# Optimization experiments

Measured on AMD Instinct MI355X. Metric: run time of the kernel, lower is better.

Reference implementation:

```python
import jax, jax.numpy as jnp
import numpy as np

B, T, C, H = 2, 2048, 1024, 16
D = C // H  # head dim = 64

def setup_inputs() -> dict:
    key = jax.random.key(0)
    ks = jax.random.split(key, 6)
    s = 0.02
    return {
        "x":  jax.random.normal(ks[0], (B, T, C), dtype=jnp.float32),
        "Wk": jax.random.normal(ks[1], (C, C), dtype=jnp.float32) * s,
        "Wq": jax.random.normal(ks[2], (C, C), dtype=jnp.float32) * s,
        "Wv": jax.random.normal(ks[3], (C, C), dtype=jnp.float32) * s,
        "Wp": jax.random.normal(ks[4], (C, C), dtype=jnp.float32) * s,
        "bp": jax.random.normal(ks[5], (C,), dtype=jnp.float32) * s,
    }

def reference(x, Wk, Wq, Wv, Wp, bp):
    Bs, Ts, Cs = x.shape
    # torch Linear: y = x @ W.T  (W is [out, in])
    def proj_heads(W):
        p = jnp.einsum('btc,dc->btd', x, W)
        return p.reshape(Bs, Ts, H, D).transpose(0, 2, 1, 3)  # [B,H,T,D]
    k = proj_heads(Wk)
    q = proj_heads(Wq)
    v = proj_heads(Wv)
    scale = 1.0 / jnp.sqrt(jnp.asarray(D, dtype=x.dtype))
    att = jnp.einsum('bhtd,bhsd->bhts', q, k) * scale  # [B,H,T,T]
    att = jax.nn.softmax(att, axis=-1)  # NOTE: no causal mask in the original forward
    y = jnp.einsum('bhts,bhsd->bhtd', att, v)
    y = y.transpose(0, 2, 1, 3).reshape(Bs, Ts, Cs)
    return jnp.einsum('btc,dc->btd', y, Wp) + bp
```

## Files before the change

### kernel.cpp

```cpp
#include <hip/hip_runtime.h>
#include <hip/hip_bf16.h>


typedef __bf16 bf16x8 __attribute__((ext_vector_type(8)));
typedef __bf16 bf16x4 __attribute__((ext_vector_type(4)));
typedef float  f32x4  __attribute__((ext_vector_type(4)));
typedef unsigned int uint2v __attribute__((ext_vector_type(2)));

#define QSCALE 0.18033688011112042f

__device__ __forceinline__ void gload_lds16(const void* g, void* l) {
  __builtin_amdgcn_global_load_lds((const __attribute__((address_space(1))) void*)g,
                                   (__attribute__((address_space(3))) void*)l, 16, 0, 0);
}
__device__ __forceinline__ unsigned int lds_off(const void* p) {
  return (unsigned int)(uintptr_t)(__attribute__((address_space(3))) const char*)p;
}
template<int IMM>
__device__ __forceinline__ uint2v tr_b64(unsigned int addr) {
  uint2v r;
  asm volatile("ds_read_b64_tr_b16 %0, %1 offset:%2" : "=v"(r) : "v"(addr), "i"(IMM));
  return r;
}

__global__ __launch_bounds__(256) void cvt_bf16(
    const float* __restrict__ x,  const float* __restrict__ wq, const float* __restrict__ wk,
    const float* __restrict__ wv, const float* __restrict__ wp,
    __bf16* __restrict__ xb,  __bf16* __restrict__ wqb, __bf16* __restrict__ wkb,
    __bf16* __restrict__ wvb, __bf16* __restrict__ wpb) {
  long long i = ((long long)blockIdx.x * 256 + threadIdx.x) * 4;
  const float* src; __bf16* dst; long long off;
  if      (i < 4194304LL) { src = x;  dst = xb;  off = i; }
  else if (i < 5242880LL) { src = wq; dst = wqb; off = i - 4194304LL; }
  else if (i < 6291456LL) { src = wk; dst = wkb; off = i - 5242880LL; }
  else if (i < 7340032LL) { src = wv; dst = wvb; off = i - 6291456LL; }
  else                    { src = wp; dst = wpb; off = i - 7340032LL; }
  float4 v = *(const float4*)(src + off);
  bf16x4 o;
  o[0] = (__bf16)v.x; o[1] = (__bf16)v.y; o[2] = (__bf16)v.z; o[3] = (__bf16)v.w;
  *(bf16x4*)(dst + off) = o;
}

__device__ __forceinline__ void gemm_core_128(
    const __bf16* __restrict__ A, const __bf16* __restrict__ Bw,
    int tileM, int tileN, char* smA, char* smB, f32x4 acc[4][4]) {
  const int tid = threadIdx.x;
  const int lane = tid & 63;
  const int wid = tid >> 6;
  const int wr = wid >> 1, wc = wid & 1;
  #pragma unroll 1
  for (int k0 = 0; k0 < 1024; k0 += 64) {
    __syncthreads();
    #pragma unroll
    for (int r = 0; r < 4; ++r) {
      int ci = tid + 256 * r;
      int row = ci >> 3, c = ci & 7;
      int sc = (c ^ (row & 7)) * 8;
      gload_lds16(A  + (long long)(tileM + row) * 1024 + k0 + sc, smA + ci * 16);
      gload_lds16(Bw + (long long)(tileN + row) * 1024 + k0 + sc, smB + ci * 16);
    }
    __syncthreads();
    #pragma unroll
    for (int kk = 0; kk < 2; ++kk) {
      bf16x8 af[4], bfr[4];
      #pragma unroll
      for (int i = 0; i < 4; ++i) {
        int mrow = wr * 64 + i * 16 + (lane & 15);
        af[i]  = *(const bf16x8*)(smA + mrow * 128 +
                   ((kk * 64 + (lane >> 4) * 16) ^ ((mrow & 7) << 4)));
        int nrow = wc * 64 + i * 16 + (lane & 15);
        bfr[i] = *(const bf16x8*)(smB + nrow * 128 +
                   ((kk * 64 + (lane >> 4) * 16) ^ ((nrow & 7) << 4)));
      }
      __builtin_amdgcn_s_setprio(1);
      #pragma unroll
      for (int mi = 0; mi < 4; ++mi)
        #pragma unroll
        for (int ni = 0; ni < 4; ++ni)
          acc[mi][ni] = __builtin_amdgcn_mfma_f32_16x16x32_bf16(af[mi], bfr[ni], acc[mi][ni], 0, 0, 0);
      __builtin_amdgcn_s_setprio(0);
    }
  }
}

__global__ __launch_bounds__(256) void gemm_qkv(
    const __bf16* __restrict__ Xb, const __bf16* __restrict__ Wqb,
    const __bf16* __restrict__ Wkb, const __bf16* __restrict__ Wvb,
    __bf16* __restrict__ Qh, __bf16* __restrict__ Kh, __bf16* __restrict__ Vh) {
  __shared__ __align__(16) char smA[16384];
  __shared__ __align__(16) char smB[16384];
  const int z = blockIdx.z;
  const __bf16* W = (z == 0) ? Wqb : (z == 1) ? Wkb : Wvb;
  __bf16* dst     = (z == 0) ? Qh  : (z == 1) ? Kh  : Vh;
  const float scale = (z == 0) ? QSCALE : 1.0f;
  const int tileM = blockIdx.x * 128, tileN = blockIdx.y * 128;
  f32x4 acc[4][4] = {};
  gemm_core_128(Xb, W, tileM, tileN, smA, smB, acc);
  const int lane = threadIdx.x & 63, wid = threadIdx.x >> 6;
  const int wr = wid >> 1, wc = wid & 1;
  #pragma unroll
  for (int mi = 0; mi < 4; ++mi) {
    #pragma unroll
    for (int ni = 0; ni < 4; ++ni) {
      int n = tileN + wc * 64 + ni * 16 + (lane & 15);
      int h = n >> 6, d = n & 63;
      #pragma unroll
      for (int r = 0; r < 4; ++r) {
        int m = tileM + wr * 64 + mi * 16 + (lane >> 4) * 4 + r;
        int b = m >> 11, t = m & 2047;
        dst[((b * 16 + h) * 2048 + t) * 64 + d] = (__bf16)(acc[mi][ni][r] * scale);
      }
    }
  }
}

__global__ __launch_bounds__(256) void gemm_proj(
    const __bf16* __restrict__ Yb, const __bf16* __restrict__ Wpb,
    const float* __restrict__ bias, float* __restrict__ out) {
  __shared__ __align__(16) char smA[16384];
  __shared__ __align__(16) char smB[16384];
  const int tileM = blockIdx.x * 128, tileN = blockIdx.y * 128;
  f32x4 acc[4][4] = {};
  gemm_core_128(Yb, Wpb, tileM, tileN, smA, smB, acc);
  const int lane = threadIdx.x & 63, wid = threadIdx.x >> 6;
  const int wr = wid >> 1, wc = wid & 1;
  #pragma unroll
  for (int mi = 0; mi < 4; ++mi) {
    #pragma unroll
    for (int ni = 0; ni < 4; ++ni) {
      int n = tileN + wc * 64 + ni * 16 + (lane & 15);
      float bv = bias[n];
      #pragma unroll
      for (int r = 0; r < 4; ++r) {
        int m = tileM + wr * 64 + mi * 16 + (lane >> 4) * 4 + r;
        out[(long long)m * 1024 + n] = acc[mi][ni][r] + bv;
      }
    }
  }
}

template<int KS>
__device__ __forceinline__ void pv_half(const char* Pw, unsigned int trb, int lane,
                                        f32x4 Oa[2][4]) {
  bf16x8 pa[2];
  #pragma unroll
  for (int mi = 0; mi < 2; ++mi) {
    int row = mi * 16 + (lane & 15);
    pa[mi] = *(const bf16x8*)(Pw + row * 128 +
               ((KS * 64 + (lane >> 4) * 16) ^ ((row & 7) << 4)));
  }
  uint2v t0[4], t1[4];
  t0[0] = tr_b64<KS * 1024 + 0 * 2048>(trb);  t1[0] = tr_b64<KS * 1024 + 0 * 2048 + 512>(trb);
  t0[1] = tr_b64<KS * 1024 + 1 * 2048>(trb);  t1[1] = tr_b64<KS * 1024 + 1 * 2048 + 512>(trb);
  t0[2] = tr_b64<KS * 1024 + 2 * 2048>(trb);  t1[2] = tr_b64<KS * 1024 + 2 * 2048 + 512>(trb);
  t0[3] = tr_b64<KS * 1024 + 3 * 2048>(trb);  t1[3] = tr_b64<KS * 1024 + 3 * 2048 + 512>(trb);
  asm volatile("s_waitcnt lgkmcnt(0)");
  __builtin_amdgcn_sched_barrier(0);
  __builtin_amdgcn_s_setprio(1);
  #pragma unroll
  for (int nd = 0; nd < 4; ++nd) {
    uint4 u; u.x = t0[nd][0]; u.y = t0[nd][1]; u.z = t1[nd][0]; u.w = t1[nd][1];
    bf16x8 vf = __builtin_bit_cast(bf16x8, u);
    #pragma unroll
    for (int mi = 0; mi < 2; ++mi)
      Oa[mi][nd] = __builtin_amdgcn_mfma_f32_16x16x32_bf16(pa[mi], vf, Oa[mi][nd], 0, 0, 0);
  }
  __builtin_amdgcn_s_setprio(0);
}

__global__ __launch_bounds__(256) void attn(
    const __bf16* __restrict__ Qh, const __bf16* __restrict__ Kh,
    const __bf16* __restrict__ Vh, float* __restrict__ Opart,
    float* __restrict__ lpart) {
  __shared__ __align__(16) char Ksm[8192];
  __shared__ __align__(16) char Vsm[8192];
  __shared__ __align__(16) char Psm[16384];
  const int tid = threadIdx.x, lane = tid & 63, wid = tid >> 6;
  const int bh = blockIdx.x;
  const int qb = blockIdx.y;
  const int split = blockIdx.z;
  const int base = bh * (2048 * 64);
  const int qrow0 = qb * 128 + wid * 32;
  const int key0 = split * 1024;

  bf16x8 qf[2][2];
  #pragma unroll
  for (int mi = 0; mi < 2; ++mi)
    #pragma unroll
    for (int kk = 0; kk < 2; ++kk)
      qf[mi][kk] = *(const bf16x8*)(Qh + base + (qrow0 + mi * 16 + (lane & 15)) * 64
                                    + kk * 32 + (lane >> 4) * 8);

  f32x4 Oa[2][4] = {};
  f32x4 lsum[2] = {};
  char* Pw = Psm + wid * 4096;
  const unsigned int trb = lds_off(Vsm) + lane * 8;

  const int kst_row = (tid + 0) >> 3;
  (void)kst_row;

  #pragma unroll 1
  for (int kt = 0; kt < 16; ++kt) {
    __syncthreads();
    #pragma unroll
    for (int r = 0; r < 2; ++r) {
      int ci = tid + 256 * r;
      int row = ci >> 3, c = ci & 7;
      int sc = (c ^ (row & 7)) * 8;
      gload_lds16(Kh + base + (key0 + kt * 64 + row) * 64 + sc, Ksm + ci * 16);
    }
    #pragma unroll
    for (int r = 0; r < 2; ++r) {
      int c = wid + 4 * r;
      int ks = c & 1, d4 = c >> 1;
      int key = ks * 32 + ((lane >> 3) & 3) * 8 + ((lane >> 5) & 1) * 4 + ((lane >> 1) & 3);
      int d = d4 * 16 + (lane & 1) * 8;
      gload_lds16(Vh + base + (key0 + kt * 64 + key) * 64 + d,
                  Vsm + ks * 1024 + d4 * 2048 + lane * 16);
    }
    __syncthreads();

    f32x4 S[2][4] = {};
    #pragma unroll
    for (int kk = 0; kk < 2; ++kk) {
      bf16x8 kf[4];
      #pragma unroll
      for (int ni = 0; ni < 4; ++ni) {
        int row = ni * 16 + (lane & 15);
        kf[ni] = *(const bf16x8*)(Ksm + row * 128 +
                   ((kk * 64 + (lane >> 4) * 16) ^ ((row & 7) << 4)));
      }
      __builtin_amdgcn_s_setprio(1);
      #pragma unroll
      for (int mi = 0; mi < 2; ++mi)
        #pragma unroll
        for (int ni = 0; ni < 4; ++ni)
          S[mi][ni] = __builtin_amdgcn_mfma_f32_16x16x32_bf16(qf[mi][kk], kf[ni], S[mi][ni], 0, 0, 0);
      __builtin_amdgcn_s_setprio(0);
    }

    #pragma unroll
    for (int mi = 0; mi < 2; ++mi) {
      #pragma unroll
      for (int ni = 0; ni < 4; ++ni) {
        f32x4 p;
        #pragma unroll
        for (int r = 0; r < 4; ++r) p[r] = exp2f(fminf(S[mi][ni][r], 60.0f));
        lsum[mi] += p;
        int key2 = (ni * 16 + (lane & 15)) * 2;
        #pragma unroll
        for (int r = 0; r < 4; ++r) {
          int row = mi * 16 + (lane >> 4) * 4 + r;
          *(__bf16*)(Pw + row * 128 + (key2 ^ ((row & 7) << 4))) = (__bf16)p[r];
        }
      }
    }

    pv_half<0>(Pw, trb, lane, Oa);
    pv_half<1>(Pw, trb, lane, Oa);
  }

  float* Op = Opart + (long long)(split * 32 + bh) * 2048 * 64;
  float* lp = lpart + (split * 32 + bh) * 2048;
  #pragma unroll
  for (int mi = 0; mi < 2; ++mi) {
    f32x4 ls = lsum[mi];
    #pragma unroll
    for (int off = 1; off < 16; off <<= 1) {
      ls[0] += __shfl_xor(ls[0], off, 64);
      ls[1] += __shfl_xor(ls[1], off, 64);
      ls[2] += __shfl_xor(ls[2], off, 64);
      ls[3] += __shfl_xor(ls[3], off, 64);
    }
    #pragma unroll
    for (int r = 0; r < 4; ++r) {
      int t = qrow0 + mi * 16 + (lane >> 4) * 4 + r;
      if ((lane & 15) == 0) lp[t] = ls[r];
      #pragma unroll
      for (int nd = 0; nd < 4; ++nd)
        Op[(long long)t * 64 + nd * 16 + (lane & 15)] = Oa[mi][nd][r];
    }
  }
}

__global__ __launch_bounds__(256) void attn_combine(
    const float* __restrict__ Opart, const float* __restrict__ lpart,
    __bf16* __restrict__ Yb) {
  int i = blockIdx.x * 256 + threadIdx.x;
  int row = i >> 4;
  int d0 = (i & 15) * 4;
  float4 o0 = *(const float4*)(Opart + (long long)row * 64 + d0);
  float4 o1 = *(const float4*)(Opart + 4194304LL + (long long)row * 64 + d0);
  float inv = 1.0f / (lpart[row] + lpart[65536 + row]);
  int bh = row >> 11, t = row & 2047;
  int b = bh >> 4, h = bh & 15;
  bf16x4 o;
  o[0] = (__bf16)((o0.x + o1.x) * inv); o[1] = (__bf16)((o0.y + o1.y) * inv);
  o[2] = (__bf16)((o0.z + o1.z) * inv); o[3] = (__bf16)((o0.w + o1.w) * inv);
  *(bf16x4*)(Yb + ((long long)(b * 2048 + t)) * 1024 + h * 64 + d0) = o;
}

extern "C" void kernel_launch(void* const* d_in, const int* in_sizes, int n_in,
                              void* d_out, int out_size, void* d_ws, size_t ws_size,
                              hipStream_t stream) {
  const float* x  = (const float*)d_in[0];
  const float* Wk = (const float*)d_in[1];
  const float* Wq = (const float*)d_in[2];
  const float* Wv = (const float*)d_in[3];
  const float* Wp = (const float*)d_in[4];
  const float* bp = (const float*)d_in[5];
  float* out = (float*)d_out;

  char* ws = (char*)d_ws;
  __bf16* Xb  = (__bf16*)ws;
  __bf16* Wqb = Xb  + 4194304;
  __bf16* Wkb = Wqb + 1048576;
  __bf16* Wvb = Wkb + 1048576;
  __bf16* Wpb = Wvb + 1048576;
  __bf16* Qh  = Wpb + 1048576;
  __bf16* Kh  = Qh  + 4194304;
  __bf16* Vh  = Kh  + 4194304;
  __bf16* Yb  = Vh  + 4194304;
  float*  Opart = (float*)(Yb + 4194304);
  float*  lpart = Opart + 8388608;

  cvt_bf16<<<8192, 256, 0, stream>>>(x, Wq, Wk, Wv, Wp, Xb, Wqb, Wkb, Wvb, Wpb);
  gemm_qkv<<<dim3(32, 8, 3), 256, 0, stream>>>(Xb, Wqb, Wkb, Wvb, Qh, Kh, Vh);
  attn<<<dim3(32, 16, 2), 256, 0, stream>>>(Qh, Kh, Vh, Opart, lpart);
  attn_combine<<<4096, 256, 0, stream>>>(Opart, lpart, Yb);
  gemm_proj<<<dim3(32, 8), 256, 0, stream>>>(Yb, Wpb, bp, out);
}
```

Before: 225.1 us.

## Double-buffer K/V tiles in attention and compute row sums via MFMA

The attention kernel now keeps two LDS buffers for K and V and prefetches the next key tile while the current one is computed, which removes one barrier per iteration and hides global load latency. P is written in a layout read back with transposed LDS reads, using packed 4-element stores instead of scalar stores. The softmax denominator is now accumulated with an extra MFMA against a ones vector, replacing the per-element adds and the final shuffle reduction. This doubles K/V shared memory, which may lower occupancy, and row sums are now taken from bf16-rounded P rather than fp32.

```diff
diff --git a/kernel.cpp b/kernel.cpp
--- a/kernel.cpp
+++ b/kernel.cpp
@@ -140,23 +140,28 @@
 }
 
 template<int KS>
-__device__ __forceinline__ void pv_half(const char* Pw, unsigned int trb, int lane,
-                                        f32x4 Oa[2][4]) {
-  bf16x8 pa[2];
-  #pragma unroll
-  for (int mi = 0; mi < 2; ++mi) {
-    int row = mi * 16 + (lane & 15);
-    pa[mi] = *(const bf16x8*)(Pw + row * 128 +
-               ((KS * 64 + (lane >> 4) * 16) ^ ((row & 7) << 4)));
-  }
+__device__ __forceinline__ void pv_half(unsigned int trP, unsigned int trV,
+                                        f32x4 Oa[2][4], f32x4 Osum[2], bf16x8 ones) {
+  uint2v pl[2], ph[2];
+  pl[0] = tr_b64<0 * 2048 + KS * 1024      >(trP);
+  ph[0] = tr_b64<0 * 2048 + KS * 1024 + 512>(trP);
+  pl[1] = tr_b64<1 * 2048 + KS * 1024      >(trP);
+  ph[1] = tr_b64<1 * 2048 + KS * 1024 + 512>(trP);
   uint2v t0[4], t1[4];
-  t0[0] = tr_b64<KS * 1024 + 0 * 2048>(trb);  t1[0] = tr_b64<KS * 1024 + 0 * 2048 + 512>(trb);
-  t0[1] = tr_b64<KS * 1024 + 1 * 2048>(trb);  t1[1] = tr_b64<KS * 1024 + 1 * 2048 + 512>(trb);
-  t0[2] = tr_b64<KS * 1024 + 2 * 2048>(trb);  t1[2] = tr_b64<KS * 1024 + 2 * 2048 + 512>(trb);
-  t0[3] = tr_b64<KS * 1024 + 3 * 2048>(trb);  t1[3] = tr_b64<KS * 1024 + 3 * 2048 + 512>(trb);
+  t0[0] = tr_b64<KS * 1024 + 0 * 2048>(trV);  t1[0] = tr_b64<KS * 1024 + 0 * 2048 + 512>(trV);
+  t0[1] = tr_b64<KS * 1024 + 1 * 2048>(trV);  t1[1] = tr_b64<KS * 1024 + 1 * 2048 + 512>(trV);
+  t0[2] = tr_b64<KS * 1024 + 2 * 2048>(trV);  t1[2] = tr_b64<KS * 1024 + 2 * 2048 + 512>(trV);
+  t0[3] = tr_b64<KS * 1024 + 3 * 2048>(trV);  t1[3] = tr_b64<KS * 1024 + 3 * 2048 + 512>(trV);
   asm volatile("s_waitcnt lgkmcnt(0)");
   __builtin_amdgcn_sched_barrier(0);
   __builtin_amdgcn_s_setprio(1);
+  bf16x8 pa[2];
+  #pragma unroll
+  for (int mi = 0; mi < 2; ++mi) {
+    uint4 u; u.x = pl[mi][0]; u.y = pl[mi][1]; u.z = ph[mi][0]; u.w = ph[mi][1];
+    pa[mi] = __builtin_bit_cast(bf16x8, u);
+    Osum[mi] = __builtin_amdgcn_mfma_f32_16x16x32_bf16(pa[mi], ones, Osum[mi], 0, 0, 0);
+  }
   #pragma unroll
   for (int nd = 0; nd < 4; ++nd) {
     uint4 u; u.x = t0[nd][0]; u.y = t0[nd][1]; u.z = t1[nd][0]; u.w = t1[nd][1];
@@ -172,8 +177,8 @@
     const __bf16* __restrict__ Qh, const __bf16* __restrict__ Kh,
     const __bf16* __restrict__ Vh, float* __restrict__ Opart,
     float* __restrict__ lpart) {
-  __shared__ __align__(16) char Ksm[8192];
-  __shared__ __align__(16) char Vsm[8192];
+  __shared__ __align__(16) char Ksm[2][8192];
+  __shared__ __align__(16) char Vsm[2][8192];
   __shared__ __align__(16) char Psm[16384];
   const int tid = threadIdx.x, lane = tid & 63, wid = tid >> 6;
   const int bh = blockIdx.x;
@@ -191,34 +196,52 @@
       qf[mi][kk] = *(const bf16x8*)(Qh + base + (qrow0 + mi * 16 + (lane & 15)) * 64
                                     + kk * 32 + (lane >> 4) * 8);
 
+  bf16x8 ones;
+  #pragma unroll
+  for (int j = 0; j < 8; ++j) ones[j] = (__bf16)1.0f;
+
   f32x4 Oa[2][4] = {};
-  f32x4 lsum[2] = {};
+  f32x4 Osum[2] = {};
   char* Pw = Psm + wid * 4096;
-  const unsigned int trb = lds_off(Vsm) + lane * 8;
-
-  const int kst_row = (tid + 0) >> 3;
-  (void)kst_row;
+  const unsigned int trP = lds_off(Psm) + wid * 4096 + lane * 8;
+
+  int ksrc[2], kdst[2], vsrc[2], vdst[2];
+  #pragma unroll
+  for (int r = 0; r < 2; ++r) {
+    int ci = tid + 256 * r;
+    int row = ci >> 3, c = ci & 7;
+    int sc = (c ^ (row & 7)) * 8;
+    ksrc[r] = base + (key0 + row) * 64 + sc;
+    kdst[r] = ci * 16;
+    int cc = wid + 4 * r;
+    int ks = cc & 1, d4 = cc >> 1;
+    int key = ks * 32 + ((lane >> 3) & 3) * 8 + ((lane >> 5) & 1) * 4 + ((lane >> 1) & 3);
+    int d = d4 * 16 + (lane & 1) * 8;
+    vsrc[r] = base + (key0 + key) * 64 + d;
+    vdst[r] = ks * 1024 + d4 * 2048 + lane * 16;
+  }
+
+  #pragma unroll
+  for (int r = 0; r < 2; ++r) {
+    gload_lds16(Kh + ksrc[r], &Ksm[0][0] + kdst[r]);
+    gload_lds16(Vh + vsrc[r], &Vsm[0][0] + vdst[r]);
+  }
+  __syncthreads();
+  int buf = 0;
 
   #pragma unroll 1
   for (int kt = 0; kt < 16; ++kt) {
-    __syncthreads();
-    #pragma unroll
-    for (int r = 0; r < 2; ++r) {
-      int ci = tid + 256 * r;
-      int row = ci >> 3, c = ci & 7;
-      int sc = (c ^ (row & 7)) * 8;
-      gload_lds16(Kh + base + (key0 + kt * 64 + row) * 64 + sc, Ksm + ci * 16);
-    }
-    #pragma unroll
-    for (int r = 0; r < 2; ++r) {
-      int c = wid + 4 * r;
-      int ks = c & 1, d4 = c >> 1;
-      int key = ks * 32 + ((lane >> 3) & 3) * 8 + ((lane >> 5) & 1) * 4 + ((lane >> 1) & 3);
-      int d = d4 * 16 + (lane & 1) * 8;
-      gload_lds16(Vh + base + (key0 + kt * 64 + key) * 64 + d,
-                  Vsm + ks * 1024 + d4 * 2048 + lane * 16);
-    }
-    __syncthreads();
+    if (kt < 15) {
+      #pragma unroll
+      for (int r = 0; r < 2; ++r) {
+        gload_lds16(Kh + ksrc[r] + (kt + 1) * 4096, &Ksm[buf ^ 1][0] + kdst[r]);
+        gload_lds16(Vh + vsrc[r] + (kt + 1) * 4096, &Vsm[buf ^ 1][0] + vdst[r]);
+      }
+    }
+    __builtin_amdgcn_sched_barrier(0);
+
+    const char* Kb = &Ksm[buf][0];
+    const unsigned int trV = lds_off(Vsm) + buf * 8192 + lane * 8;
 
     f32x4 S[2][4] = {};
     #pragma unroll
@@ -227,7 +250,7 @@
       #pragma unroll
       for (int ni = 0; ni < 4; ++ni) {
         int row = ni * 16 + (lane & 15);
-        kf[ni] = *(const bf16x8*)(Ksm + row * 128 +
+        kf[ni] = *(const bf16x8*)(Kb + row * 128 +
                    ((kk * 64 + (lane >> 4) * 16) ^ ((row & 7) << 4)));
       }
       __builtin_amdgcn_s_setprio(1);
@@ -243,39 +266,30 @@
     for (int mi = 0; mi < 2; ++mi) {
       #pragma unroll
       for (int ni = 0; ni < 4; ++ni) {
-        f32x4 p;
+        bf16x4 pb;
         #pragma unroll
-        for (int r = 0; r < 4; ++r) p[r] = exp2f(fminf(S[mi][ni][r], 60.0f));
-        lsum[mi] += p;
-        int key2 = (ni * 16 + (lane & 15)) * 2;
-        #pragma unroll
-        for (int r = 0; r < 4; ++r) {
-          int row = mi * 16 + (lane >> 4) * 4 + r;
-          *(__bf16*)(Pw + row * 128 + (key2 ^ ((row & 7) << 4))) = (__bf16)p[r];
-        }
-      }
-    }
-
-    pv_half<0>(Pw, trb, lane, Oa);
-    pv_half<1>(Pw, trb, lane, Oa);
+        for (int r = 0; r < 4; ++r) pb[r] = (__bf16)exp2f(fminf(S[mi][ni][r], 60.0f));
+        int kq = ni * 16 + (lane & 15);
+        *(bf16x4*)(Pw + mi * 2048 + (kq >> 5) * 1024 + ((kq >> 2) & 1) * 512 +
+                   ((kq >> 3) & 3) * 128 + (kq & 3) * 32 + (lane >> 4) * 8) = pb;
+      }
+    }
+
+    pv_half<0>(trP, trV, Oa, Osum, ones);
+    pv_half<1>(trP, trV, Oa, Osum, ones);
+
+    __syncthreads();
+    buf ^= 1;
   }
 
   float* Op = Opart + (long long)(split * 32 + bh) * 2048 * 64;
   float* lp = lpart + (split * 32 + bh) * 2048;
   #pragma unroll
   for (int mi = 0; mi < 2; ++mi) {
-    f32x4 ls = lsum[mi];
-    #pragma unroll
-    for (int off = 1; off < 16; off <<= 1) {
-      ls[0] += __shfl_xor(ls[0], off, 64);
-      ls[1] += __shfl_xor(ls[1], off, 64);
-      ls[2] += __shfl_xor(ls[2], off, 64);
-      ls[3] += __shfl_xor(ls[3], off, 64);
-    }
     #pragma unroll
     for (int r = 0; r < 4; ++r) {
       int t = qrow0 + mi * 16 + (lane >> 4) * 4 + r;
-      if ((lane & 15) == 0) lp[t] = ls[r];
+      if ((lane & 15) == 0) lp[t] = Osum[mi][r];
       #pragma unroll
       for (int nd = 0; nd < 4; ++nd)
         Op[(long long)t * 64 + nd * 16 + (lane & 15)] = Oa[mi][nd][r];
```

Result: faster. 208.5 us (-7.4%).
